# Optimization experiments

Measured on AMD Instinct MI355X. Metric: run time of the kernel, lower is better.

The kernel has to match this reference:

```python
import jax, jax.numpy as jnp
import numpy as np

B, S, DIM = 2, 2048, 2048
H = 16
Q_LORA, KV_LORA = 768, 512
NOPE, ROPE, VD = 128, 64, 128
QKD = NOPE + ROPE  # 192
SOFTCAP = 30.0
EPS = 1e-6
NEG = -1e9
SCALE = QKD ** -0.5  # max_seq_len <= original_seq_len -> no mscale correction


def rms_norm(x, w, eps=EPS):
    xf = x.astype(jnp.float32)
    y = xf * jax.lax.rsqrt(jnp.mean(xf * xf, axis=-1, keepdims=True) + eps)
    return (y * w.astype(jnp.float32)).astype(x.dtype)


def apply_rope(x, cos, sin):
    # x: [B, S, H, D] with interleaved (even, odd) pairs; cos/sin: [S, D//2]
    xr = x.astype(jnp.float32).reshape(*x.shape[:-1], -1, 2)
    xe, xo = xr[..., 0], xr[..., 1]
    c = cos[None, :, None, :]
    s = sin[None, :, None, :]
    ye = xe * c - xo * s
    yo = xe * s + xo * c
    return jnp.stack([ye, yo], axis=-1).reshape(x.shape).astype(x.dtype)


def setup_inputs():
    key = jax.random.key(0)
    ks = jax.random.split(key, 6)
    def w(k, shape, fan_in):
        return jax.random.normal(k, shape, jnp.float32) * (fan_in ** -0.5)
    x = jax.random.normal(ks[0], (B, S, DIM), jnp.float32)
    wq_a_w = w(ks[1], (Q_LORA, DIM), DIM)
    wq_b_w = w(ks[2], (H * QKD, Q_LORA), Q_LORA)
    wkv_a_w = w(ks[3], (KV_LORA + ROPE, DIM), DIM)
    wkv_b_w = w(ks[4], (H * (NOPE + VD), KV_LORA), KV_LORA)
    wo_w = w(ks[5], (DIM, H * VD), H * VD)
    q_norm_w = jnp.ones((Q_LORA,), jnp.float32)
    kv_norm_w = jnp.ones((KV_LORA,), jnp.float32)
    q_gain = jnp.full((H,), 1.5, jnp.float32)  # qk_gain_init
    inv_freq = 1.0 / (10000.0 ** (np.arange(0, ROPE, 2, dtype=np.float32) / ROPE))
    fr = np.outer(np.arange(S, dtype=np.float32), inv_freq)  # [S, 32]
    freqs_cos = jnp.asarray(np.cos(fr))
    freqs_sin = jnp.asarray(np.sin(fr))
    mask = jnp.asarray(np.where(np.triu(np.ones((S, S), dtype=bool), 1), NEG, 0.0).astype(np.float32))
    return dict(x=x, wq_a_w=wq_a_w, q_norm_w=q_norm_w, wq_b_w=wq_b_w, q_gain=q_gain,
                wkv_a_w=wkv_a_w, kv_norm_w=kv_norm_w, wkv_b_w=wkv_b_w, wo_w=wo_w,
                freqs_cos=freqs_cos, freqs_sin=freqs_sin, mask=mask, start_pos=0)


def reference(x, wq_a_w, q_norm_w, wq_b_w, q_gain, wkv_a_w, kv_norm_w, wkv_b_w, wo_w,
              freqs_cos, freqs_sin, mask, start_pos):
    b, s, _ = x.shape
    # low-rank Q: wq_a -> RMSNorm -> wq_b
    q = rms_norm(x @ wq_a_w.T, q_norm_w) @ wq_b_w.T          # [B,S,H*QKD]
    q = q.reshape(b, s, H, QKD)
    q_nope, q_pe = q[..., :NOPE], q[..., NOPE:]
    q_pe = apply_rope(q_pe, freqs_cos, freqs_sin)            # rope_dims=0 -> full 64-dim rotation
    q_pe = q_pe * q_gain[None, None, :, None]                # learned per-head QK gain
    # low-rank KV + decoupled rope key
    kv_full = x @ wkv_a_w.T                                  # [B,S,KV_LORA+ROPE]
    kv, k_pe = kv_full[..., :KV_LORA], kv_full[..., KV_LORA:]
    kv = rms_norm(kv, kv_norm_w)
    k_pe = apply_rope(k_pe[:, :, None, :], freqs_cos, freqs_sin)  # [B,S,1,ROPE]
    # prefill (mask is not None) branch: expand latent kv through wkv_b
    kvb = (kv @ wkv_b_w.T).reshape(b, s, H, NOPE + VD)
    k_nope, v = kvb[..., :NOPE], kvb[..., NOPE:]
    k = jnp.concatenate([k_nope, jnp.broadcast_to(k_pe, (b, s, H, ROPE))], axis=-1)
    qf = jnp.concatenate([q_nope, q_pe], axis=-1)            # [B,S,H,QKD]
    scores = jnp.einsum('bshd,bthd->bsht', qf, k) * SCALE
    scores = SOFTCAP * jnp.tanh(scores / SOFTCAP)            # logit softcap
    scores = scores + mask[None, :, None, :]                 # causal additive mask [S,T]
    p = jax.nn.softmax(scores.astype(jnp.float32), axis=-1).astype(x.dtype)
    y = jnp.einsum('bsht,bthd->bshd', p, v)                  # [B,S,H,VD]
    # XSA: subtract self-value projection
    vn = v * jax.lax.rsqrt(jnp.maximum(jnp.sum(v * v, axis=-1, keepdims=True), 1e-12))
    y = y - jnp.sum(y * vn, axis=-1, keepdims=True) * vn
    return y.reshape(b, s, H * VD) @ wo_w.T                  # [B,S,DIM]
```

## Files before the change

kernel.cpp:

```cpp
#include <hip/hip_runtime.h>
#include <stdint.h>

typedef unsigned short u16;
typedef __bf16 bf16x8 __attribute__((ext_vector_type(8)));
typedef float f32x4 __attribute__((ext_vector_type(4)));
typedef unsigned int u32x4 __attribute__((ext_vector_type(4)));
typedef unsigned int u32x2 __attribute__((ext_vector_type(2)));

typedef __attribute__((address_space(3))) void LDSV;
typedef __attribute__((address_space(1))) void GLV;

#define S_LEN 2048

__device__ __forceinline__ float bf2f(u16 u) {
  union { unsigned int i; float f; } v; v.i = ((unsigned int)u) << 16; return v.f;
}
__device__ __forceinline__ u16 f2bf(float f) {
  union { float f; unsigned int i; } v; v.f = f;
  unsigned int x = v.i;
  return (u16)((x + 0x7fffu + ((x >> 16) & 1u)) >> 16);
}
__device__ __forceinline__ unsigned int cvtpk(float lo, float hi) {
  unsigned int r;
  asm("v_cvt_pk_bf16_f32 %0, %1, %2" : "=v"(r) : "v"(lo), "v"(hi));
  return r;
}
__device__ __forceinline__ unsigned long long pack4(float4 v) {
  return (unsigned long long)f2bf(v.x)
       | ((unsigned long long)f2bf(v.y) << 16)
       | ((unsigned long long)f2bf(v.z) << 32)
       | ((unsigned long long)f2bf(v.w) << 48);
}

__global__ __launch_bounds__(256) void cast_all(
    const float* __restrict__ s0, u16* __restrict__ d0, long e0,
    const float* __restrict__ s1, u16* __restrict__ d1, long e1,
    const float* __restrict__ s2, u16* __restrict__ d2, long e2,
    const float* __restrict__ s3, u16* __restrict__ d3, long e3,
    const float* __restrict__ s4, u16* __restrict__ d4, long e4,
    const float* __restrict__ s5, u16* __restrict__ d5, long e5) {
  long i = (long)blockIdx.x * 256 + threadIdx.x;
  const float* src; u16* dst; long base; bool pad = false;
  if (i < e0)      { src = s0; dst = d0; base = 0; }
  else if (i < e1) { src = s1; dst = d1; base = e0; }
  else if (i < e2) { src = s2; dst = d2; base = e1; }
  else if (i < e3) { src = s3; dst = d3; base = e2; }
  else if (i < e4) { src = s4; dst = d4; base = e3; }
  else if (i < e5) { src = s5; dst = d5; base = e4; pad = true; }
  else return;
  long li = i - base;
  long elem0 = li * 4;
  unsigned long long r = 0;
  if (!pad || (elem0 >> 11) < 576)
    r = pack4(*(const float4*)(src + elem0));
  ((unsigned long long*)dst)[li] = r;
}

#define MM_PHASE(QM, QN, BB)                                                     \
  __builtin_amdgcn_s_setprio(1);                                                 \
  {                                                                              \
    _Pragma("unroll") for (int mf = 0; mf < 4; ++mf) {                           \
      _Pragma("unroll") for (int nf = 0; nf < 2; ++nf) {                         \
        _Pragma("unroll") for (int kk = 0; kk < 2; ++kk) {                       \
          acc[(QM) * 4 + mf][(QN) * 2 + nf] =                                    \
              __builtin_amdgcn_mfma_f32_16x16x32_bf16(                           \
                  a[mf][kk], BB[nf][kk], acc[(QM) * 4 + mf][(QN) * 2 + nf],      \
                  0, 0, 0);                                                      \
        }                                                                        \
      }                                                                          \
    }                                                                            \
  }                                                                              \
  __builtin_amdgcn_s_setprio(0);

__global__ __launch_bounds__(512, 2) void gemm256_dual(const u16* __restrict__ Aq,
                                                       const u16* __restrict__ Bq,
                                                       u16* __restrict__ Cq,
                                                       const u16* __restrict__ Akv,
                                                       const u16* __restrict__ Bkv,
                                                       u16* __restrict__ KbN,
                                                       u16* __restrict__ Vc) {
  __shared__ u16 SMEM[65536];
  const int tid = threadIdx.x;
  const int lane = tid & 63, wid = tid >> 6;
  const int l15 = lane & 15, l4 = lane >> 4;
  const int wm16 = (wid >> 2) * 16, wn16 = (wid & 3) * 16;

  const int id = blockIdx.x;
  const bool m0 = (id < 192);
  const u16* A = m0 ? Aq : Akv;
  const u16* B = m0 ? Bq : Bkv;
  const int lda = 1408;
  const int ldb = m0 ? 768 : 512;
  const int K   = m0 ? 768 : 512;
  const int gx  = m0 ? 12 : 16;
  const int nwg = m0 ? 192 : 256;
  const int lin0 = m0 ? id : id - 192;
  const int cpx = nwg >> 3;
  const int swzb = (lin0 & 7) * cpx + (lin0 >> 3);
  const long bm = (long)(swzb / gx) * 256;
  const long bn = (long)(swzb % gx) * 256;

  long aoff[2], boff[2];
#pragma unroll
  for (int j = 0; j < 2; ++j) {
    int lb = (j * 512 + tid) * 16;
    int swz = lb ^ (((lb >> 7) & 7) << 4);
    int sr = swz >> 7, sc = (swz & 127) >> 1;
    aoff[j] = (bm + sr) * (long)lda + sc;
    boff[j] = (bn + sr) * (long)ldb + sc;
  }

  auto STAGE = [&](int buf, int half, int isB, int tt) {
#pragma unroll
    for (int j = 0; j < 2; ++j) {
      const u16* src = isB ? (B + boff[j] + (long)half * 128 * ldb + tt * 64)
                           : (A + aoff[j] + (long)half * 128 * lda + tt * 64);
      __builtin_amdgcn_global_load_lds(
          (const GLV*)src,
          (LDSV*)((char*)SMEM + isB * 65536 + buf * 32768 + half * 16384 +
                  (j * 512 + tid) * 16),
          16, 0, 0);
    }
  };

  f32x4 acc[8][4] = {};
  bf16x8 a[4][2], b0[2][2], b1[2][2];

  auto LDA_ = [&](int buf, int qm) {
#pragma unroll
    for (int mf = 0; mf < 4; ++mf)
#pragma unroll
      for (int kk = 0; kk < 2; ++kk) {
        int r = mf * 32 + wm16 + l15;
        int lb = r * 128 + kk * 64 + l4 * 16;
        a[mf][kk] = *(const bf16x8*)((char*)SMEM + buf * 32768 + qm * 16384 +
                                     (lb ^ ((r & 7) << 4)));
      }
  };
  auto LDB_ = [&](int buf, int qn, bf16x8 (*bb)[2]) {
#pragma unroll
    for (int nf = 0; nf < 2; ++nf)
#pragma unroll
      for (int kk = 0; kk < 2; ++kk) {
        int r = nf * 64 + wn16 + l15;
        int lb = r * 128 + kk * 64 + l4 * 16;
        bb[nf][kk] = *(const bf16x8*)((char*)SMEM + 65536 + buf * 32768 +
                                      qn * 16384 + (lb ^ ((r & 7) << 4)));
      }
  };

  const int NT = K >> 6;
  STAGE(0, 0, 0, 0); STAGE(0, 0, 1, 0); STAGE(0, 1, 1, 0); STAGE(0, 1, 0, 0);
  STAGE(1, 0, 0, 1); STAGE(1, 0, 1, 1);
  asm volatile("s_waitcnt vmcnt(4)" ::: "memory");
  __builtin_amdgcn_s_barrier();

  for (int t = 0; t < NT; ++t) {
    const int cb = t & 1;
    if (t + 1 < NT) STAGE(cb ^ 1, 1, 1, t + 1);
    LDA_(cb, 0);
    LDB_(cb, 0, b0);
    __builtin_amdgcn_s_barrier();
    asm volatile("s_waitcnt lgkmcnt(0)" ::: "memory");
    __builtin_amdgcn_sched_barrier(0);
    MM_PHASE(0, 0, b0);
    __builtin_amdgcn_s_barrier();
    if (t + 1 < NT) STAGE(cb ^ 1, 1, 0, t + 1);
    LDB_(cb, 1, b1);
    __builtin_amdgcn_s_barrier();
    asm volatile("s_waitcnt lgkmcnt(0)" ::: "memory");
    __builtin_amdgcn_sched_barrier(0);
    MM_PHASE(0, 1, b1);
    __builtin_amdgcn_s_barrier();
    if (t + 2 < NT) STAGE(cb, 0, 0, t + 2);
    LDA_(cb, 1);
    __builtin_amdgcn_s_barrier();
    asm volatile("s_waitcnt lgkmcnt(0)" ::: "memory");
    __builtin_amdgcn_sched_barrier(0);
    MM_PHASE(1, 0, b0);
    __builtin_amdgcn_s_barrier();
    if (t + 2 < NT) STAGE(cb, 0, 1, t + 2);
    __builtin_amdgcn_s_barrier();
    MM_PHASE(1, 1, b1);
    if (t + 2 < NT) asm volatile("s_waitcnt vmcnt(4)" ::: "memory");
    else            asm volatile("s_waitcnt vmcnt(0)" ::: "memory");
    __builtin_amdgcn_s_barrier();
  }

#pragma unroll
  for (int mfg = 0; mfg < 8; ++mfg)
#pragma unroll
    for (int nfg = 0; nfg < 4; ++nfg)
#pragma unroll
      for (int r = 0; r < 4; ++r) {
        long row = bm + mfg * 32 + wm16 + l4 * 4 + r;
        long col = bn + nfg * 64 + wn16 + l15;
        float v = acc[mfg][nfg][r];
        if (m0) {
          Cq[row * 3072 + col] = f2bf(v);
        } else {
          int h = (int)(col >> 8), c = (int)(col & 255);
          if (c < 128)
            KbN[(((row >> 11) * 16 + h) * 2048 + (row & 2047)) * 128 + c] = f2bf(v);
          else
            Vc[row * 2048 + h * 128 + (c - 128)] = f2bf(v);
        }
      }
}

#define MM_TALL(QM, QN, BB)                                                      \
  __builtin_amdgcn_s_setprio(1);                                                 \
  {                                                                              \
    _Pragma("unroll") for (int mf = 0; mf < 4; ++mf) {                           \
      _Pragma("unroll") for (int kk = 0; kk < 2; ++kk) {                         \
        acc[(QM) * 4 + mf][(QN)] = __builtin_amdgcn_mfma_f32_16x16x32_bf16(      \
            a[mf][kk], BB[kk], acc[(QM) * 4 + mf][(QN)], 0, 0, 0);               \
      }                                                                          \
    }                                                                            \
  }                                                                              \
  __builtin_amdgcn_s_setprio(0);

template <int MODE>
__global__ __launch_bounds__(512, 2) void gemm_tall(const u16* __restrict__ A, int lda,
                                                    const u16* __restrict__ B, int ldb,
                                                    void* __restrict__ Cv, int ldc,
                                                    u16* __restrict__ Vc, int K) {
  __shared__ u16 SMEM[49152];
  const int tid = threadIdx.x;
  const int lane = tid & 63, wid = tid >> 6;
  const int l15 = lane & 15, l4 = lane >> 4;
  const int wm16 = (wid >> 2) * 16, wn16 = (wid & 3) * 16;

  const int gx = gridDim.x, nwg = gx * gridDim.y;
  int lin0 = blockIdx.y * gx + blockIdx.x;
  int cpx = nwg >> 3;
  int swzb = (lin0 & 7) * cpx + (lin0 >> 3);
  const long bm = (long)(swzb / gx) * 256;
  const long bn = (long)(swzb % gx) * 128;

  long aoff[2], boffv;
#pragma unroll
  for (int j = 0; j < 2; ++j) {
    int lb = (j * 512 + tid) * 16;
    int swz = lb ^ (((lb >> 7) & 7) << 4);
    aoff[j] = (bm + (swz >> 7)) * (long)lda + ((swz & 127) >> 1);
  }
  {
    int lb = tid * 16;
    int swz = lb ^ (((lb >> 7) & 7) << 4);
    boffv = (bn + (swz >> 7)) * (long)ldb + ((swz & 127) >> 1);
  }

  auto SA = [&](int buf, int half, int tt) {
#pragma unroll
    for (int j = 0; j < 2; ++j)
      __builtin_amdgcn_global_load_lds(
          (const GLV*)(A + aoff[j] + (long)half * 128 * lda + tt * 64),
          (LDSV*)((char*)SMEM + buf * 32768 + half * 16384 + (j * 512 + tid) * 16),
          16, 0, 0);
  };
  auto SB = [&](int buf, int half, int tt) {
    __builtin_amdgcn_global_load_lds(
        (const GLV*)(B + boffv + (long)half * 64 * ldb + tt * 64),
        (LDSV*)((char*)SMEM + 65536 + buf * 16384 + half * 8192 + tid * 16),
        16, 0, 0);
  };

  f32x4 acc[8][2] = {};
  bf16x8 a[4][2], b0[2], b1[2];

  auto LDA_ = [&](int buf, int qm) {
#pragma unroll
    for (int mf = 0; mf < 4; ++mf)
#pragma unroll
      for (int kk = 0; kk < 2; ++kk) {
        int r = mf * 32 + wm16 + l15;
        int lb = r * 128 + kk * 64 + l4 * 16;
        a[mf][kk] = *(const bf16x8*)((char*)SMEM + buf * 32768 + qm * 16384 +
                                     (lb ^ ((r & 7) << 4)));
      }
  };
  auto LDB_ = [&](int buf, int qn, bf16x8* bb) {
#pragma unroll
    for (int kk = 0; kk < 2; ++kk) {
      int r = wn16 + l15;
      int lb = r * 128 + kk * 64 + l4 * 16;
      bb[kk] = *(const bf16x8*)((char*)SMEM + 65536 + buf * 16384 + qn * 8192 +
                                (lb ^ ((r & 7) << 4)));
    }
  };

  const int NT = K >> 6;
  SA(0, 0, 0); SB(0, 0, 0); SB(0, 1, 0); SA(0, 1, 0);
  SA(1, 0, 1); SB(1, 0, 1);
  asm volatile("s_waitcnt vmcnt(3)" ::: "memory");
  __builtin_amdgcn_s_barrier();

  for (int t = 0; t < NT; ++t) {
    const int cb = t & 1;
    if (t + 1 < NT) SB(cb ^ 1, 1, t + 1);
    LDA_(cb, 0);
    LDB_(cb, 0, b0);
    __builtin_amdgcn_s_barrier();
    asm volatile("s_waitcnt lgkmcnt(0)" ::: "memory");
    __builtin_amdgcn_sched_barrier(0);
    MM_TALL(0, 0, b0);
    __builtin_amdgcn_s_barrier();
    if (t + 1 < NT) SA(cb ^ 1, 1, t + 1);
    LDB_(cb, 1, b1);
    __builtin_amdgcn_s_barrier();
    asm volatile("s_waitcnt lgkmcnt(0)" ::: "memory");
    __builtin_amdgcn_sched_barrier(0);
    MM_TALL(0, 1, b1);
    __builtin_amdgcn_s_barrier();
    if (t + 2 < NT) SA(cb, 0, t + 2);
    LDA_(cb, 1);
    __builtin_amdgcn_s_barrier();
    asm volatile("s_waitcnt lgkmcnt(0)" ::: "memory");
    __builtin_amdgcn_sched_barrier(0);
    MM_TALL(1, 0, b0);
    __builtin_amdgcn_s_barrier();
    if (t + 2 < NT) SB(cb, 0, t + 2);
    __builtin_amdgcn_s_barrier();
    MM_TALL(1, 1, b1);
    if (t + 2 < NT) asm volatile("s_waitcnt vmcnt(6)" ::: "memory");
    else            asm volatile("s_waitcnt vmcnt(0)" ::: "memory");
    __builtin_amdgcn_s_barrier();
  }

#pragma unroll
  for (int mfg = 0; mfg < 8; ++mfg)
#pragma unroll
    for (int qn = 0; qn < 2; ++qn)
#pragma unroll
      for (int r = 0; r < 4; ++r) {
        long row = bm + mfg * 32 + wm16 + l4 * 4 + r;
        long col = bn + qn * 64 + wn16 + l15;
        float v = acc[mfg][qn][r];
        if constexpr (MODE == 0) {
          ((u16*)Cv)[row * ldc + col] = f2bf(v);
        } else {
          ((float*)Cv)[row * ldc + col] = v;
        }
      }
}

__global__ __launch_bounds__(256) void rmsnorm2_kernel(u16* __restrict__ qakv,
                                                       const float* __restrict__ qw,
                                                       const float* __restrict__ kvw,
                                                       const float* __restrict__ cosb,
                                                       const float* __restrict__ sinb,
                                                       u16* __restrict__ kpe) {
  __shared__ float sred[4];
  const int tid = threadIdx.x;
  const int row = blockIdx.x;
  if (row < 4096) {
    u16* p = qakv + (size_t)row * 1408;
    float x[3];
    float ss = 0.f;
#pragma unroll
    for (int i = 0; i < 3; ++i) { x[i] = bf2f(p[tid + i * 256]); ss += x[i] * x[i]; }
#pragma unroll
    for (int off = 1; off < 64; off <<= 1) ss += __shfl_xor(ss, off);
    if ((tid & 63) == 0) sred[tid >> 6] = ss;
    __syncthreads();
    float tot = sred[0] + sred[1] + sred[2] + sred[3];
    float rs = rsqrtf(tot * (1.0f / 768.0f) + 1e-6f) * 0.0069411711f;
#pragma unroll
    for (int i = 0; i < 3; ++i) p[tid + i * 256] = f2bf(x[i] * rs * qw[tid + i * 256]);
  } else {
    const int srow = row - 4096;
    u16* p = qakv + (size_t)srow * 1408 + 768;
    float x[2];
    float ss = 0.f;
#pragma unroll
    for (int i = 0; i < 2; ++i) { x[i] = bf2f(p[tid + i * 256]); ss += x[i] * x[i]; }
#pragma unroll
    for (int off = 1; off < 64; off <<= 1) ss += __shfl_xor(ss, off);
    if ((tid & 63) == 0) sred[tid >> 6] = ss;
    __syncthreads();
    float tot = sred[0] + sred[1] + sred[2] + sred[3];
    float rs = rsqrtf(tot * (1.0f / 512.0f) + 1e-6f);
#pragma unroll
    for (int i = 0; i < 2; ++i) p[tid + i * 256] = f2bf(x[i] * rs * kvw[tid + i * 256]);
    if (tid < 32) {
      int s = srow & 2047;
      unsigned int v = *(const unsigned int*)(qakv + (size_t)srow * 1408 + 1280 + 2 * tid);
      float xe = bf2f((u16)(v & 0xffff)), xo = bf2f((u16)(v >> 16));
      float c = cosb[s * 32 + tid], sn = sinb[s * 32 + tid];
      *(unsigned int*)(kpe + (size_t)srow * 64 + 2 * tid) =
          (unsigned int)f2bf(xe * c - xo * sn) | ((unsigned int)f2bf(xe * sn + xo * c) << 16);
    }
  }
}

__global__ __launch_bounds__(256) void v_transpose_kernel(const u16* __restrict__ Vc,
                                                          u16* __restrict__ VT) {
  __shared__ u16 tile[64][65];
  int bh = blockIdx.z;
  int d0 = blockIdx.y * 64;
  int t0 = blockIdx.x * 64;
  int b = bh >> 4, h = bh & 15;
#pragma unroll
  for (int i = 0; i < 2; ++i) {
    int flat = i * 256 + threadIdx.x;
    int t = flat >> 3, c = (flat & 7) * 8;
    u32x4 v = *(const u32x4*)(Vc + ((long)b * S_LEN + t0 + t) * 2048 + h * 128 + d0 + c);
    const u16* pv = (const u16*)&v;
#pragma unroll
    for (int j = 0; j < 8; ++j) tile[c + j][t] = pv[j];
  }
  __syncthreads();
#pragma unroll
  for (int i = 0; i < 2; ++i) {
    int flat = i * 256 + threadIdx.x;
    int d = flat >> 3, tc = (flat & 7) * 8;
    u32x4 v;
    u16* pv = (u16*)&v;
#pragma unroll
    for (int j = 0; j < 8; ++j) pv[j] = tile[d][tc + j];
    *(u32x4*)(VT + ((long)bh * 128 + d0 + d) * S_LEN + t0 + tc) = v;
  }
}

__global__ __launch_bounds__(512, 2) void attn_kernel(const u16* __restrict__ Qg,
                                                      const u16* __restrict__ KbN,
                                                      const u16* __restrict__ Kpe,
                                                      const u16* __restrict__ VTg,
                                                      const u16* __restrict__ Vcg,
                                                      const float* __restrict__ cosb,
                                                      const float* __restrict__ sinb,
                                                      const float* __restrict__ gain,
                                                      u16* __restrict__ Yg) {
  __shared__ u16 Ks[2][64 * 192];
  __shared__ u16 VTs[2][128 * 64];
  __shared__ u16 Ps[128 * 64];

  const int tid = threadIdx.x, lane = tid & 63, wid = tid >> 6;
  const int l15 = lane & 15, l4 = lane >> 4;

  const int p = blockIdx.x;
  const int bh = (p & 7) * 4 + (p >> 6);
  const int pair = (p >> 3) & 7;
  const int b = bh >> 4, h = bh & 15;

  const u16* Kn = KbN + (long)bh * S_LEN * 128;
  const u16* Kp = Kpe + (long)b * S_LEN * 64;
  const u16* Vbh = VTg + (long)bh * 128 * S_LEN;

  int krow[3], sst[3], ksoff[3];
  const u16* sb[3];
#pragma unroll
  for (int i = 0; i < 3; ++i) {
    int flat = i * 512 + tid;
    int r = flat / 24, c = flat % 24;
    krow[i] = r;
    if (c < 16) { sb[i] = Kn + c * 8; sst[i] = 128; }
    else        { sb[i] = Kp + (c - 16) * 8; sst[i] = 64; }
    ksoff[i] = r * 192 + ((c ^ (r & 7)) * 8);
  }
  int vrow[2], vc[2], vsoff[2];
#pragma unroll
  for (int i = 0; i < 2; ++i) {
    int flat = i * 512 + tid;
    vrow[i] = flat >> 3; vc[i] = flat & 7;
    vsoff[i] = vrow[i] * 64 + ((vc[i] ^ (vrow[i] & 7)) * 8);
  }

  const int prow = wid * 16 + l15;
  const int pr7 = prow & 7;
  const float g = gain[h];

  for (int seg = 0; seg < 2; ++seg) {
    const int qt = seg ? pair : 15 - pair;
    const int q0 = qt * 128;
    const int nkt = 2 * qt + 2;
    const int sq = q0 + prow;

    bf16x8 qf[6];
    {
      const u16* qb_ = Qg + ((long)b * S_LEN + sq) * 3072 + h * 192;
#pragma unroll
      for (int f = 0; f < 6; ++f) qf[f] = *(const bf16x8*)(qb_ + f * 32 + 8 * l4);
    }
#pragma unroll
    for (int f = 4; f < 6; ++f) {
      float4 cv = *(const float4*)(cosb + sq * 32 + (f - 4) * 16 + l4 * 4);
      float4 sv = *(const float4*)(sinb + sq * 32 + (f - 4) * 16 + l4 * 4);
      float cc[4] = {cv.x, cv.y, cv.z, cv.w};
      float ssn[4] = {sv.x, sv.y, sv.z, sv.w};
      u16* pq = (u16*)&qf[f];
#pragma unroll
      for (int pp = 0; pp < 4; ++pp) {
        float xe = bf2f(pq[2 * pp]), xo = bf2f(pq[2 * pp + 1]);
        pq[2 * pp]     = f2bf((xe * cc[pp] - xo * ssn[pp]) * g);
        pq[2 * pp + 1] = f2bf((xe * ssn[pp] + xo * cc[pp]) * g);
      }
    }

    f32x4 o[8] = {};
    float lsum = 0.f;

    u32x4 ka[3], va[2];
#pragma unroll
    for (int i = 0; i < 3; ++i)
      ka[i] = *(const u32x4*)(sb[i] + (long)krow[i] * sst[i]);
#pragma unroll
    for (int i = 0; i < 2; ++i)
      va[i] = *(const u32x4*)(Vbh + (long)vrow[i] * S_LEN + vc[i] * 8);
#pragma unroll
    for (int i = 0; i < 3; ++i) *(u32x4*)(&Ks[0][ksoff[i]]) = ka[i];
#pragma unroll
    for (int i = 0; i < 2; ++i) *(u32x4*)(&VTs[0][vsoff[i]]) = va[i];
    if (nkt > 1) {
#pragma unroll
      for (int i = 0; i < 3; ++i)
        ka[i] = *(const u32x4*)(sb[i] + (long)(64 + krow[i]) * sst[i]);
#pragma unroll
      for (int i = 0; i < 2; ++i)
        va[i] = *(const u32x4*)(Vbh + (long)vrow[i] * S_LEN + 64 + vc[i] * 8);
    }
    __syncthreads();

    for (int it = 0; it < nkt; ++it) {
      const int cur = it & 1;

      f32x4 sacc[4] = {};
      __builtin_amdgcn_s_setprio(1);
#pragma unroll
      for (int f = 0; f < 6; ++f)
#pragma unroll
        for (int tf = 0; tf < 4; ++tf) {
          int row = tf * 16 + l15;
          bf16x8 kf = *(const bf16x8*)(&Ks[cur][row * 192 + (((f * 4 + l4) ^ (row & 7)) * 8)]);
          sacc[tf] = __builtin_amdgcn_mfma_f32_16x16x32_bf16(kf, qf[f], sacc[tf], 0, 0, 0);
        }
      __builtin_amdgcn_s_setprio(0);

      if (it + 1 < nkt) {
#pragma unroll
        for (int i = 0; i < 3; ++i) *(u32x4*)(&Ks[cur ^ 1][ksoff[i]]) = ka[i];
#pragma unroll
        for (int i = 0; i < 2; ++i) *(u32x4*)(&VTs[cur ^ 1][vsoff[i]]) = va[i];
      }
      if (it + 2 < nkt) {
        int k0n = (it + 2) * 64;
#pragma unroll
        for (int i = 0; i < 3; ++i)
          ka[i] = *(const u32x4*)(sb[i] + (long)(k0n + krow[i]) * sst[i]);
#pragma unroll
        for (int i = 0; i < 2; ++i)
          va[i] = *(const u32x4*)(Vbh + (long)vrow[i] * S_LEN + k0n + vc[i] * 8);
      }

#pragma unroll
      for (int tf = 0; tf < 4; ++tf)
#pragma unroll
        for (int r = 0; r < 4; ++r) {
          float u = __builtin_amdgcn_exp2f(sacc[tf][r]);
          sacc[tf][r] = __builtin_amdgcn_exp2f(-86.56170245333781f *
                                               __builtin_amdgcn_rcpf(u + 1.0f));
        }
      if (it * 64 >= q0) {
        const int dthr = q0 + prow - it * 64 - l4 * 4;
#pragma unroll
        for (int tf = 0; tf < 4; ++tf)
#pragma unroll
          for (int r = 0; r < 4; ++r)
            if (tf * 16 + r > dthr) sacc[tf][r] = 0.f;
      }
#pragma unroll
      for (int tf = 0; tf < 4; ++tf)
#pragma unroll
        for (int r = 0; r < 4; ++r) lsum += sacc[tf][r];

#pragma unroll
      for (int tf = 0; tf < 4; ++tf) {
        u32x2 w;
        w.x = cvtpk(sacc[tf][0], sacc[tf][1]);
        w.y = cvtpk(sacc[tf][2], sacc[tf][3]);
        int chunk = tf * 2 + (l4 >> 1);
        *(u32x2*)(&Ps[prow * 64 + ((chunk ^ pr7) * 8) + (l4 & 1) * 4]) = w;
      }

      __builtin_amdgcn_s_setprio(1);
#pragma unroll
      for (int kk = 0; kk < 2; ++kk) {
        bf16x8 pf = *(const bf16x8*)(&Ps[prow * 64 + (((kk * 4 + l4) ^ pr7) * 8)]);
#pragma unroll
        for (int nf = 0; nf < 8; ++nf) {
          int vr = nf * 16 + l15;
          bf16x8 vf = *(const bf16x8*)(&VTs[cur][vr * 64 + (((kk * 4 + l4) ^ (vr & 7)) * 8)]);
          o[nf] = __builtin_amdgcn_mfma_f32_16x16x32_bf16(pf, vf, o[nf], 0, 0, 0);
        }
      }
      __builtin_amdgcn_s_setprio(0);

      __syncthreads();
    }

    lsum += __shfl_xor(lsum, 16);
    lsum += __shfl_xor(lsum, 32);
    float inv[4];
#pragma unroll
    for (int r = 0; r < 4; ++r)
      inv[r] = __builtin_amdgcn_rcpf(__shfl(lsum, l4 * 4 + r));

    float yv[8][4], vvv[8][4];
    float ssum[4] = {0.f, 0.f, 0.f, 0.f}, dsum[4] = {0.f, 0.f, 0.f, 0.f};
    const u16* vb = Vcg + ((long)b * S_LEN + q0 + wid * 16) * 2048 + h * 128;
#pragma unroll
    for (int nf = 0; nf < 8; ++nf)
#pragma unroll
      for (int r = 0; r < 4; ++r) {
        float vv = bf2f(vb[(l4 * 4 + r) * 2048 + nf * 16 + l15]);
        float y = o[nf][r] * inv[r];
        vvv[nf][r] = vv; yv[nf][r] = y;
        ssum[r] += vv * vv; dsum[r] += y * vv;
      }
#pragma unroll
    for (int r = 0; r < 4; ++r) {
      ssum[r] += __shfl_xor(ssum[r], 1); ssum[r] += __shfl_xor(ssum[r], 2);
      ssum[r] += __shfl_xor(ssum[r], 4); ssum[r] += __shfl_xor(ssum[r], 8);
      dsum[r] += __shfl_xor(dsum[r], 1); dsum[r] += __shfl_xor(dsum[r], 2);
      dsum[r] += __shfl_xor(dsum[r], 4); dsum[r] += __shfl_xor(dsum[r], 8);
      dsum[r] *= __builtin_amdgcn_rcpf(fmaxf(ssum[r], 1e-12f));
    }
#pragma unroll
    for (int nf = 0; nf < 8; ++nf)
#pragma unroll
      for (int r = 0; r < 4; ++r) {
        long row = (long)b * S_LEN + q0 + wid * 16 + l4 * 4 + r;
        Yg[row * 2048 + h * 128 + nf * 16 + l15] = f2bf(yv[nf][r] - dsum[r] * vvv[nf][r]);
      }
  }
}

extern "C" void kernel_launch(void* const* d_in, const int* in_sizes, int n_in,
                              void* d_out, int out_size, void* d_ws, size_t ws_size,
                              hipStream_t stream) {
  const float* x       = (const float*)d_in[0];
  const float* wq_a    = (const float*)d_in[1];
  const float* q_norm  = (const float*)d_in[2];
  const float* wq_b    = (const float*)d_in[3];
  const float* q_gain  = (const float*)d_in[4];
  const float* wkv_a   = (const float*)d_in[5];
  const float* kv_norm = (const float*)d_in[6];
  const float* wkv_b   = (const float*)d_in[7];
  const float* wo      = (const float*)d_in[8];
  const float* fcos    = (const float*)d_in[9];
  const float* fsin    = (const float*)d_in[10];
  float* out = (float*)d_out;

  char* ws = (char*)d_ws;
  size_t off = 0;
  auto alloc = [&](size_t bytes) {
    char* pp = ws + off;
    off += (bytes + 255) & ~(size_t)255;
    return pp;
  };
  const long M = 4096;
  u16* xb    = (u16*)alloc(M * 2048 * 2);
  u16* wcomb = (u16*)alloc(1408L * 2048 * 2);
  u16* wqbb  = (u16*)alloc(3072L * 768 * 2);
  u16* wkvbb = (u16*)alloc(4096L * 512 * 2);
  u16* wob   = (u16*)alloc(2048L * 2048 * 2);
  u16* qakv  = (u16*)alloc(M * 1408 * 2);
  u16* qb    = (u16*)alloc(M * 3072 * 2);
  u16* KbN   = (u16*)alloc(32L * 2048 * 128 * 2);
  u16* kpe   = (u16*)alloc(M * 64 * 2);
  u16* Vc    = (u16*)alloc(M * 2048 * 2);
  u16* VTb   = (u16*)alloc(32L * 128 * 2048 * 2);
  u16* Yb    = (u16*)alloc(M * 2048 * 2);

  const long n4_x = 2097152, n4_wqa = 393216, n4_wqb = 589824,
             n4_wkvb = 524288, n4_wo = 1048576, n4_wkvap = 327680;
  long e0 = n4_x, e1 = e0 + n4_wqa, e2 = e1 + n4_wqb, e3 = e2 + n4_wkvb,
       e4 = e3 + n4_wo, e5 = e4 + n4_wkvap;
  cast_all<<<(int)(e5 / 256), 256, 0, stream>>>(
      x, xb, e0, wq_a, wcomb, e1, wq_b, wqbb, e2, wkv_b, wkvbb, e3,
      wo, wob, e4, wkv_a, wcomb + 768L * 2048, e5);

  gemm_tall<0><<<dim3(11, 16), 512, 0, stream>>>(xb, 2048, wcomb, 2048, qakv, 1408, nullptr, 2048);
  rmsnorm2_kernel<<<8192, 256, 0, stream>>>(qakv, q_norm, kv_norm, fcos, fsin, kpe);
  gemm256_dual<<<448, 512, 0, stream>>>(qakv, wqbb, qb, qakv + 768, wkvbb, KbN, Vc);
  v_transpose_kernel<<<dim3(32, 2, 32), 256, 0, stream>>>(Vc, VTb);
  attn_kernel<<<256, 512, 0, stream>>>(qb, KbN, kpe, VTb, Vc, fcos, fsin, q_gain, Yb);
  gemm_tall<1><<<dim3(16, 16), 512, 0, stream>>>(Yb, 2048, wob, 2048, out, 2048, nullptr, 2048);
}
```

Baseline: 234.6 us.

## Fuse V transpose into attention kernel via scattered LDS writes

```diff
diff --git a/kernel.cpp b/kernel.cpp
--- a/kernel.cpp
+++ b/kernel.cpp
@@ -394,39 +394,9 @@
   }
 }
 
-__global__ __launch_bounds__(256) void v_transpose_kernel(const u16* __restrict__ Vc,
-                                                          u16* __restrict__ VT) {
-  __shared__ u16 tile[64][65];
-  int bh = blockIdx.z;
-  int d0 = blockIdx.y * 64;
-  int t0 = blockIdx.x * 64;
-  int b = bh >> 4, h = bh & 15;
-#pragma unroll
-  for (int i = 0; i < 2; ++i) {
-    int flat = i * 256 + threadIdx.x;
-    int t = flat >> 3, c = (flat & 7) * 8;
-    u32x4 v = *(const u32x4*)(Vc + ((long)b * S_LEN + t0 + t) * 2048 + h * 128 + d0 + c);
-    const u16* pv = (const u16*)&v;
-#pragma unroll
-    for (int j = 0; j < 8; ++j) tile[c + j][t] = pv[j];
-  }
-  __syncthreads();
-#pragma unroll
-  for (int i = 0; i < 2; ++i) {
-    int flat = i * 256 + threadIdx.x;
-    int d = flat >> 3, tc = (flat & 7) * 8;
-    u32x4 v;
-    u16* pv = (u16*)&v;
-#pragma unroll
-    for (int j = 0; j < 8; ++j) pv[j] = tile[d][tc + j];
-    *(u32x4*)(VT + ((long)bh * 128 + d0 + d) * S_LEN + t0 + tc) = v;
-  }
-}
-
 __global__ __launch_bounds__(512, 2) void attn_kernel(const u16* __restrict__ Qg,
                                                       const u16* __restrict__ KbN,
                                                       const u16* __restrict__ Kpe,
-                                                      const u16* __restrict__ VTg,
                                                       const u16* __restrict__ Vcg,
                                                       const float* __restrict__ cosb,
                                                       const float* __restrict__ sinb,
@@ -446,7 +416,7 @@
 
   const u16* Kn = KbN + (long)bh * S_LEN * 128;
   const u16* Kp = Kpe + (long)b * S_LEN * 64;
-  const u16* Vbh = VTg + (long)bh * 128 * S_LEN;
+  const u16* Vcb = Vcg + ((long)b * S_LEN) * 2048 + h * 128;
 
   int krow[3], sst[3], ksoff[3];
   const u16* sb[3];
@@ -459,12 +429,14 @@
     else        { sb[i] = Kp + (c - 16) * 8; sst[i] = 64; }
     ksoff[i] = r * 192 + ((c ^ (r & 7)) * 8);
   }
-  int vrow[2], vc[2], vsoff[2];
+  int vt_[2], vdc[2], vA0[2], vs0[2];
 #pragma unroll
   for (int i = 0; i < 2; ++i) {
     int flat = i * 512 + tid;
-    vrow[i] = flat >> 3; vc[i] = flat & 7;
-    vsoff[i] = vrow[i] * 64 + ((vc[i] ^ (vrow[i] & 7)) * 8);
+    int t = flat >> 4, dc = flat & 15;
+    vt_[i] = t; vdc[i] = dc;
+    vA0[i] = dc * 512 + (t & 7);
+    vs0[i] = (t >> 3) ^ (dc & 7);
   }
 
   const int prow = wid * 16 + l15;
@@ -502,23 +474,31 @@
     float lsum = 0.f;
 
     u32x4 ka[3], va[2];
+    auto VWRITE = [&](int buf) {
+#pragma unroll
+      for (int i = 0; i < 2; ++i) {
+        const u16* pv = (const u16*)&va[i];
+#pragma unroll
+        for (int j = 0; j < 8; ++j)
+          VTs[buf][vA0[i] + j * 64 + ((vs0[i] ^ j) << 3)] = pv[j];
+      }
+    };
 #pragma unroll
     for (int i = 0; i < 3; ++i)
       ka[i] = *(const u32x4*)(sb[i] + (long)krow[i] * sst[i]);
 #pragma unroll
     for (int i = 0; i < 2; ++i)
-      va[i] = *(const u32x4*)(Vbh + (long)vrow[i] * S_LEN + vc[i] * 8);
+      va[i] = *(const u32x4*)(Vcb + (long)vt_[i] * 2048 + vdc[i] * 8);
 #pragma unroll
     for (int i = 0; i < 3; ++i) *(u32x4*)(&Ks[0][ksoff[i]]) = ka[i];
-#pragma unroll
-    for (int i = 0; i < 2; ++i) *(u32x4*)(&VTs[0][vsoff[i]]) = va[i];
+    VWRITE(0);
     if (nkt > 1) {
 #pragma unroll
       for (int i = 0; i < 3; ++i)
         ka[i] = *(const u32x4*)(sb[i] + (long)(64 + krow[i]) * sst[i]);
 #pragma unroll
       for (int i = 0; i < 2; ++i)
-        va[i] = *(const u32x4*)(Vbh + (long)vrow[i] * S_LEN + 64 + vc[i] * 8);
+        va[i] = *(const u32x4*)(Vcb + (long)(64 + vt_[i]) * 2048 + vdc[i] * 8);
     }
     __syncthreads();
 
@@ -540,8 +520,7 @@
       if (it + 1 < nkt) {
 #pragma unroll
         for (int i = 0; i < 3; ++i) *(u32x4*)(&Ks[cur ^ 1][ksoff[i]]) = ka[i];
-#pragma unroll
-        for (int i = 0; i < 2; ++i) *(u32x4*)(&VTs[cur ^ 1][vsoff[i]]) = va[i];
+        VWRITE(cur ^ 1);
       }
       if (it + 2 < nkt) {
         int k0n = (it + 2) * 64;
@@ -550,7 +529,7 @@
           ka[i] = *(const u32x4*)(sb[i] + (long)(k0n + krow[i]) * sst[i]);
 #pragma unroll
         for (int i = 0; i < 2; ++i)
-          va[i] = *(const u32x4*)(Vbh + (long)vrow[i] * S_LEN + k0n + vc[i] * 8);
+          va[i] = *(const u32x4*)(Vcb + (long)(k0n + vt_[i]) * 2048 + vdc[i] * 8);
       }
 
 #pragma unroll
@@ -590,7 +569,8 @@
 #pragma unroll
         for (int nf = 0; nf < 8; ++nf) {
           int vr = nf * 16 + l15;
-          bf16x8 vf = *(const bf16x8*)(&VTs[cur][vr * 64 + (((kk * 4 + l4) ^ (vr & 7)) * 8)]);
+          int cc = (kk * 4 + l4) ^ (vr & 7) ^ ((vr >> 3) & 7);
+          bf16x8 vf = *(const bf16x8*)(&VTs[cur][vr * 64 + cc * 8]);
           o[nf] = __builtin_amdgcn_mfma_f32_16x16x32_bf16(pf, vf, o[nf], 0, 0, 0);
         }
       }
@@ -670,7 +650,6 @@
   u16* KbN   = (u16*)alloc(32L * 2048 * 128 * 2);
   u16* kpe   = (u16*)alloc(M * 64 * 2);
   u16* Vc    = (u16*)alloc(M * 2048 * 2);
-  u16* VTb   = (u16*)alloc(32L * 128 * 2048 * 2);
   u16* Yb    = (u16*)alloc(M * 2048 * 2);
 
   const long n4_x = 2097152, n4_wqa = 393216, n4_wqb = 589824,
@@ -684,7 +663,6 @@
   gemm_tall<0><<<dim3(11, 16), 512, 0, stream>>>(xb, 2048, wcomb, 2048, qakv, 1408, nullptr, 2048);
   rmsnorm2_kernel<<<8192, 256, 0, stream>>>(qakv, q_norm, kv_norm, fcos, fsin, kpe);
   gemm256_dual<<<448, 512, 0, stream>>>(qakv, wqbb, qb, qakv + 768, wkvbb, KbN, Vc);
-  v_transpose_kernel<<<dim3(32, 2, 32), 256, 0, stream>>>(Vc, VTb);
-  attn_kernel<<<256, 512, 0, stream>>>(qb, KbN, kpe, VTb, Vc, fcos, fsin, q_gain, Yb);
+  attn_kernel<<<256, 512, 0, stream>>>(qb, KbN, kpe, Vc, fcos, fsin, q_gain, Yb);
   gemm_tall<1><<<dim3(16, 16), 512, 0, stream>>>(Yb, 2048, wob, 2048, out, 2048, nullptr, 2048);
 }
```

Measured after the change: 247.2 us. +5.4%, slower.
